# Kernel optimization log

Hardware: AMD Instinct MI355X
Metric: run time of the kernel (lower is better)

## Reference

```python
import jax, jax.numpy as jnp
import numpy as np

NEG_SLOPE = 0.2


def _gat_layer(x, src, dst, W, att_src, att_dst, bias, concat):
    # x: [N, Fin], W: [Fin, H*C], att_*: [H, C], bias: [H*C] or [C]
    N = x.shape[0]
    H, C = att_src.shape
    h = (x @ W).reshape(N, H, C)                      # node features per head
    a_src = jnp.sum(h * att_src, axis=-1)             # [N, H]
    a_dst = jnp.sum(h * att_dst, axis=-1)             # [N, H]
    e = jax.nn.leaky_relu(a_src[src] + a_dst[dst], NEG_SLOPE)  # [E, H]
    # segment softmax over destination nodes
    m = jax.ops.segment_max(e, dst, num_segments=N)   # [N, H]
    m = jnp.where(jnp.isfinite(m), m, 0.0)
    ex = jnp.exp(e - m[dst])
    s = jax.ops.segment_sum(ex, dst, num_segments=N)  # [N, H]
    alpha = ex / (s[dst] + 1e-16)                     # [E, H]
    msg = h[src] * alpha[:, :, None]                  # [E, H, C]
    out = jax.ops.segment_sum(msg, dst, num_segments=N)  # [N, H, C]
    out = out.reshape(N, H * C) if concat else out.mean(axis=1)
    return out + bias


def setup_inputs() -> dict:
    key = jax.random.key(0)
    ks = jax.random.split(key, 20)
    N, E, Fin, Cg, H = 50000, 800000, 128, 64, 4
    HC = H * Cg
    s = 0.1
    x = jax.random.normal(ks[0], (N, Fin), jnp.float32)
    edge_index = jax.random.randint(ks[1], (2, E), 0, N, dtype=jnp.int32)
    inp = {
        'x': x,
        'edge_index': edge_index,
        'W0': jax.random.normal(ks[2], (Fin, HC), jnp.float32) * s,
        'as0': jax.random.normal(ks[3], (H, Cg), jnp.float32) * s,
        'ad0': jax.random.normal(ks[4], (H, Cg), jnp.float32) * s,
        'b0': jnp.zeros((HC,), jnp.float32),
        'W1': jax.random.normal(ks[5], (HC, HC), jnp.float32) * s,
        'as1': jax.random.normal(ks[6], (H, Cg), jnp.float32) * s,
        'ad1': jax.random.normal(ks[7], (H, Cg), jnp.float32) * s,
        'b1': jnp.zeros((HC,), jnp.float32),
        'W2': jax.random.normal(ks[8], (HC, HC), jnp.float32) * s,
        'as2': jax.random.normal(ks[9], (H, Cg), jnp.float32) * s,
        'ad2': jax.random.normal(ks[10], (H, Cg), jnp.float32) * s,
        'b2': jnp.zeros((Cg,), jnp.float32),
        # linear head: 64 -> 128 -> 10
        'lw0': jax.random.normal(ks[11], (Cg, 128), jnp.float32) * s,
        'lb0': jnp.zeros((128,), jnp.float32),
        'lw1': jax.random.normal(ks[12], (128, 10), jnp.float32) * s,
        'lb1': jnp.zeros((10,), jnp.float32),
    }
    return inp


def reference(x, edge_index, W0, as0, ad0, b0, W1, as1, ad1, b1,
              W2, as2, ad2, b2, lw0, lb0, lw1, lb1):
    N = x.shape[0]
    # PyG GATConv add_self_loops=True: append self-loop edges
    loop = jnp.arange(N, dtype=edge_index.dtype)
    src = jnp.concatenate([edge_index[0], loop])
    dst = jnp.concatenate([edge_index[1], loop])
    h = _gat_layer(x, src, dst, W0, as0, ad0, b0, True)
    h = _gat_layer(h, src, dst, W1, as1, ad1, b1, True)
    h = _gat_layer(h, src, dst, W2, as2, ad2, b2, False)
    h = jax.nn.relu(h @ lw0 + lb0)
    return h @ lw1 + lb1
```

## Files before the change

kernel.cpp:

```cpp
#include <hip/hip_runtime.h>
#include <hip/hip_bf16.h>

#define HEADS 4
#define CH 64
#define HC 256

typedef __attribute__((ext_vector_type(8))) short short8;
typedef __attribute__((ext_vector_type(4))) float f32x4;
typedef __attribute__((ext_vector_type(8))) _Float16 half8;

__device__ inline unsigned short f2bf(float f){
  unsigned u = __float_as_uint(f);
  return (unsigned short)((u + 0x7FFF + ((u >> 16) & 1)) >> 16);
}


__global__ void hist_kernel(const int* __restrict__ dst, int E, int ET, int* __restrict__ cnt){
  int e = blockIdx.x * blockDim.x + threadIdx.x;
  if (e >= ET) return;
  int d = (e < E) ? dst[e] : (e - E);
  atomicAdd(&cnt[d], 1);
}

__global__ void blocksum_kernel(const int* __restrict__ cnt, int N, int* __restrict__ bsum){
  int tid = threadIdx.x;
  int i = blockIdx.x * 256 + tid;
  int v = (i < N) ? cnt[i] : 0;
  #pragma unroll
  for (int off = 32; off >= 1; off >>= 1) v += __shfl_xor(v, off);
  __shared__ int ws[4];
  if ((tid & 63) == 0) ws[tid >> 6] = v;
  __syncthreads();
  if (tid == 0) bsum[blockIdx.x] = ws[0] + ws[1] + ws[2] + ws[3];
}

__global__ void scanb_kernel(int* __restrict__ bsum, int nb){
  __shared__ int buf[256];
  int tid = threadIdx.x;
  int v = (tid < nb) ? bsum[tid] : 0;
  buf[tid] = v;
  __syncthreads();
  #pragma unroll
  for (int off = 1; off < 256; off <<= 1){
    int t = (tid >= off) ? buf[tid - off] : 0;
    __syncthreads();
    buf[tid] += t;
    __syncthreads();
  }
  if (tid < nb) bsum[tid] = buf[tid] - v;
}

__global__ void scanfinal_kernel(const int* __restrict__ cnt, const int* __restrict__ bsum,
                                 int* __restrict__ ptr, int* __restrict__ cur, int N){
  __shared__ int buf[256];
  int tid = threadIdx.x;
  int i = blockIdx.x * 256 + tid;
  int v = (i < N) ? cnt[i] : 0;
  buf[tid] = v;
  __syncthreads();
  #pragma unroll
  for (int off = 1; off < 256; off <<= 1){
    int t = (tid >= off) ? buf[tid - off] : 0;
    __syncthreads();
    buf[tid] += t;
    __syncthreads();
  }
  int exc = buf[tid] - v + bsum[blockIdx.x];
  if (i < N){
    ptr[i] = exc; cur[i] = exc;
    if (i == N - 1) ptr[N] = exc + v;
  }
}

__global__ void scatter_kernel(const int* __restrict__ src, const int* __restrict__ dst,
                               int E, int ET, int* __restrict__ cur,
                               int* __restrict__ csr_src, int* __restrict__ csr_dst){
  int e = blockIdx.x * blockDim.x + threadIdx.x;
  if (e >= ET) return;
  int s, d;
  if (e < E){ s = src[e]; d = dst[e]; } else { s = e - E; d = e - E; }
  int pos = atomicAdd(&cur[d], 1);
  csr_src[pos] = s;
  csr_dst[pos] = d;
}


__global__ void dhist_kernel(const int* __restrict__ cnt, int N, int* __restrict__ dbins){
  __shared__ int lb[64];
  int tid = threadIdx.x;
  if (tid < 64) lb[tid] = 0;
  __syncthreads();
  int n = blockIdx.x * 256 + tid;
  if (n < N) atomicAdd(&lb[min(cnt[n], 63)], 1);
  __syncthreads();
  if (tid < 64 && lb[tid]) atomicAdd(&dbins[tid], lb[tid]);
}

__global__ void dscan_kernel(int* __restrict__ dbins, int* __restrict__ dcur){
  int lane = threadIdx.x;
  int v = dbins[lane];
  int s = v;
  #pragma unroll
  for (int off = 1; off < 64; off <<= 1){
    int t = __shfl_up(s, off);
    if (lane >= off) s += t;
  }
  int exc = s - v;
  dbins[lane] = exc;
  dcur[lane] = exc;
}

__global__ void dscatter_kernel(const int* __restrict__ cnt, int N, int* __restrict__ dcur,
                                int* __restrict__ perm){
  __shared__ int lb[64];
  __shared__ int base[64];
  int tid = threadIdx.x;
  if (tid < 64) lb[tid] = 0;
  __syncthreads();
  int n = blockIdx.x * 256 + tid;
  bool valid = n < N;
  int bin = 0, rank = 0;
  if (valid){
    bin = min(cnt[n], 63);
    rank = atomicAdd(&lb[bin], 1);
  }
  __syncthreads();
  if (tid < 64) base[tid] = lb[tid] ? atomicAdd(&dcur[tid], lb[tid]) : 0;
  __syncthreads();
  if (valid) perm[base[bin] + rank] = n;
}


__global__ void ew_kernel(const int* __restrict__ csr_src, const int* __restrict__ csr_dst,
                          const float* __restrict__ a_src, const float* __restrict__ a_dst,
                          float* __restrict__ w, int ET){
  int i = blockIdx.x * 256 + threadIdx.x;
  if (i >= ET) return;
  int s = csr_src[i], d = csr_dst[i];
  float4 as = *(const float4*)&a_src[(size_t)s * 4];
  float4 ad = *(const float4*)&a_dst[(size_t)d * 4];
  float4 r;
  float e;
  e = as.x + ad.x; e = e > 0.f ? e : 0.2f * e; r.x = __expf(e);
  e = as.y + ad.y; e = e > 0.f ? e : 0.2f * e; r.y = __expf(e);
  e = as.z + ad.z; e = e > 0.f ? e : 0.2f * e; r.z = __expf(e);
  e = as.w + ad.w; e = e > 0.f ? e : 0.2f * e; r.w = __expf(e);
  *(float4*)&w[(size_t)i * 4] = r;
}


__global__ void wsplit_kernel(const float* __restrict__ W0, unsigned short* __restrict__ h0,
                              unsigned short* __restrict__ l0,
                              const float* __restrict__ W1, unsigned short* __restrict__ h1,
                              unsigned short* __restrict__ l1,
                              const float* __restrict__ W2, unsigned short* __restrict__ h2,
                              unsigned short* __restrict__ l2){
  int idx = blockIdx.x * 256 + threadIdx.x;
  const float* W; unsigned short *hi, *lo; int K;
  if (idx < 128 * HC){ W = W0; hi = h0; lo = l0; K = 128; }
  else if (idx < (128 + 256) * HC){ idx -= 128 * HC; W = W1; hi = h1; lo = l1; K = 256; }
  else { idx -= (128 + 256) * HC; W = W2; hi = h2; lo = l2; K = 256; }
  int k = idx >> 8, n = idx & 255;
  float w = W[idx];
  unsigned short hb = f2bf(w);
  float hf = __uint_as_float((unsigned)hb << 16);
  unsigned short lb = f2bf(w - hf);
  hi[(size_t)n * K + k] = hb;
  lo[(size_t)n * K + k] = lb;
}


__global__ void xsplit_kernel(const float* __restrict__ x, int total4,
                              unsigned short* __restrict__ xhi, unsigned short* __restrict__ xlo){
  int i4 = blockIdx.x * 256 + threadIdx.x;
  if (i4 >= total4) return;
  float4 v = *(const float4*)&x[(size_t)i4 * 4];
  float va[4] = {v.x, v.y, v.z, v.w};
  unsigned short h4[4], l4[4];
  #pragma unroll
  for (int j = 0; j < 4; j++){
    unsigned short hb = f2bf(va[j]);
    float hf = __uint_as_float((unsigned)hb << 16);
    h4[j] = hb;
    l4[j] = f2bf(va[j] - hf);
  }
  *(ushort4*)&xhi[(size_t)i4 * 4] = make_ushort4(h4[0], h4[1], h4[2], h4[3]);
  *(ushort4*)&xlo[(size_t)i4 * 4] = make_ushort4(l4[0], l4[1], l4[2], l4[3]);
}


__global__ void lwsplit_kernel(const float* __restrict__ lw0,
                               unsigned short* __restrict__ l0hi, unsigned short* __restrict__ l0lo,
                               const float* __restrict__ lw1, _Float16* __restrict__ l1T){
  int idx = blockIdx.x * 256 + threadIdx.x;
  if (idx < 8192){
    int n = idx & 127, k = idx >> 7;
    float w = lw0[k * 128 + n];
    unsigned short hb = f2bf(w);
    float hf = __uint_as_float((unsigned)hb << 16);
    unsigned short lb = f2bf(w - hf);
    l0hi[n * 64 + k] = hb;
    l0lo[n * 64 + k] = lb;
  } else if (idx < 8192 + 2048){
    int id = idx - 8192;
    int n = id & 15, k = id >> 4;
    float w = (n < 10) ? lw1[k * 10 + n] : 0.f;
    l1T[n * 128 + k] = (_Float16)w;
  }
}


__launch_bounds__(256, 2)
__global__ void gemm_mfma_kernel(const unsigned short* __restrict__ Ahi,
                                 const unsigned short* __restrict__ Alo,
                                 const unsigned short* __restrict__ BhiT,
                                 const unsigned short* __restrict__ BloT,
                                 _Float16* __restrict__ Cm,
                                 const float* __restrict__ att_s, const float* __restrict__ att_d,
                                 float* __restrict__ a_src, float* __restrict__ a_dst,
                                 int K){
  __shared__ unsigned short As_hi[128][40];
  __shared__ unsigned short As_lo[128][40];
  __shared__ unsigned short Bs_hi[128][40];
  __shared__ unsigned short Bs_lo[128][40];

  int tid = threadIdx.x;
  int m0 = blockIdx.x * 128, n0 = blockIdx.y * 128;
  int wave = tid >> 6, lane = tid & 63;
  int wm = (wave >> 1) * 64, wn = (wave & 1) * 64;
  int col = lane & 15, quad = lane >> 4;

  int mS = tid >> 2, q8 = (tid & 3) * 8;
  size_t baseA0 = (size_t)(m0 + mS) * K + q8;
  size_t baseA1 = (size_t)(m0 + mS + 64) * K + q8;
  size_t baseB0 = (size_t)(n0 + mS) * K + q8;
  size_t baseB1 = (size_t)(n0 + mS + 64) * K + q8;

  short8 pA[4], pB[4];
  pA[0] = *(const short8*)&Ahi[baseA0];  pA[1] = *(const short8*)&Alo[baseA0];
  pA[2] = *(const short8*)&Ahi[baseA1];  pA[3] = *(const short8*)&Alo[baseA1];
  pB[0] = *(const short8*)&BhiT[baseB0]; pB[1] = *(const short8*)&BloT[baseB0];
  pB[2] = *(const short8*)&BhiT[baseB1]; pB[3] = *(const short8*)&BloT[baseB1];

  f32x4 acc[4][4];
  #pragma unroll
  for (int a = 0; a < 4; a++)
    #pragma unroll
    for (int b = 0; b < 4; b++)
      acc[a][b] = (f32x4){0.f, 0.f, 0.f, 0.f};

  for (int k0 = 0; k0 < K; k0 += 32){
    __syncthreads();
    *(short8*)&As_hi[mS][q8]      = pA[0];
    *(short8*)&As_lo[mS][q8]      = pA[1];
    *(short8*)&As_hi[mS + 64][q8] = pA[2];
    *(short8*)&As_lo[mS + 64][q8] = pA[3];
    *(short8*)&Bs_hi[mS][q8]      = pB[0];
    *(short8*)&Bs_lo[mS][q8]      = pB[1];
    *(short8*)&Bs_hi[mS + 64][q8] = pB[2];
    *(short8*)&Bs_lo[mS + 64][q8] = pB[3];
    __syncthreads();

    if (k0 + 32 < K){
      size_t o = (size_t)(k0 + 32);
      pA[0] = *(const short8*)&Ahi[baseA0 + o];  pA[1] = *(const short8*)&Alo[baseA0 + o];
      pA[2] = *(const short8*)&Ahi[baseA1 + o];  pA[3] = *(const short8*)&Alo[baseA1 + o];
      pB[0] = *(const short8*)&BhiT[baseB0 + o]; pB[1] = *(const short8*)&BloT[baseB0 + o];
      pB[2] = *(const short8*)&BhiT[baseB1 + o]; pB[3] = *(const short8*)&BloT[baseB1 + o];
    }

    short8 af[4][2], bf[4][2];
    #pragma unroll
    for (int t = 0; t < 4; t++){
      af[t][0] = *(const short8*)&As_hi[wm + t * 16 + col][quad * 8];
      af[t][1] = *(const short8*)&As_lo[wm + t * 16 + col][quad * 8];
      bf[t][0] = *(const short8*)&Bs_hi[wn + t * 16 + col][quad * 8];
      bf[t][1] = *(const short8*)&Bs_lo[wn + t * 16 + col][quad * 8];
    }
    #pragma unroll
    for (int mt = 0; mt < 4; mt++)
      #pragma unroll
      for (int nt = 0; nt < 4; nt++){
        acc[mt][nt] = __builtin_amdgcn_mfma_f32_16x16x32_bf16(af[mt][0], bf[nt][0], acc[mt][nt], 0, 0, 0);
        acc[mt][nt] = __builtin_amdgcn_mfma_f32_16x16x32_bf16(af[mt][1], bf[nt][0], acc[mt][nt], 0, 0, 0);
        acc[mt][nt] = __builtin_amdgcn_mfma_f32_16x16x32_bf16(af[mt][0], bf[nt][1], acc[mt][nt], 0, 0, 0);
      }
  }

  #pragma unroll
  for (int mt = 0; mt < 4; mt++)
    #pragma unroll
    for (int nt = 0; nt < 4; nt++){
      int colg = n0 + wn + nt * 16 + col;
      #pragma unroll
      for (int r = 0; r < 4; r++){
        int row = m0 + wm + mt * 16 + quad * 4 + r;
        Cm[(size_t)row * HC + colg] = (_Float16)acc[mt][nt][r];
      }
    }

  int head = (n0 + wn) >> 6;
  float asv[4], adv[4];
  #pragma unroll
  for (int nt = 0; nt < 4; nt++){
    asv[nt] = att_s[head * CH + nt * 16 + col];
    adv[nt] = att_d[head * CH + nt * 16 + col];
  }
  #pragma unroll
  for (int mt = 0; mt < 4; mt++){
    float sp[4] = {0.f,0.f,0.f,0.f}, dp[4] = {0.f,0.f,0.f,0.f};
    #pragma unroll
    for (int nt = 0; nt < 4; nt++)
      #pragma unroll
      for (int r = 0; r < 4; r++){
        sp[r] += acc[mt][nt][r] * asv[nt];
        dp[r] += acc[mt][nt][r] * adv[nt];
      }
    #pragma unroll
    for (int off = 1; off <= 8; off <<= 1)
      #pragma unroll
      for (int r = 0; r < 4; r++){
        sp[r] += __shfl_xor(sp[r], off);
        dp[r] += __shfl_xor(dp[r], off);
      }
    if (col == 0){
      #pragma unroll
      for (int r = 0; r < 4; r++){
        int row = m0 + wm + mt * 16 + quad * 4 + r;
        a_src[row * HEADS + head] = sp[r];
        a_dst[row * HEADS + head] = dp[r];
      }
    }
  }
}


__global__ void agg_kernel(const _Float16* __restrict__ h, const float* __restrict__ w,
                           const int* __restrict__ ptr, const int* __restrict__ csr_src,
                           const int* __restrict__ perm,
                           const float* __restrict__ bias,
                           unsigned short* __restrict__ out_hi, unsigned short* __restrict__ out_lo,
                           int mean_mode, const float* __restrict__ b2,
                           float* __restrict__ f2){
  __shared__ float sm[HEADS][8][CH];
  int head = threadIdx.x >> 6;
  int lane = threadIdx.x & 63;
  int slot = lane >> 3, c8 = lane & 7;
  int pn = perm[blockIdx.x * 8 + slot];
  int beg = 0, deg = 0;
  if (pn >= 0){ beg = ptr[pn]; deg = ptr[pn + 1] - beg; }

  int maxdeg = deg;
  #pragma unroll
  for (int off = 8; off <= 32; off <<= 1) maxdeg = max(maxdeg, __shfl_xor(maxdeg, off));

  float acc[8] = {0.f,0.f,0.f,0.f,0.f,0.f,0.f,0.f};
  float ss = 0.f;
  #pragma unroll 2
  for (int it = 0; it < maxdeg; ++it){
    bool valid = it < deg;
    int idx = beg + (valid ? it : 0);
    int s = csr_src[idx];
    float wv = w[(size_t)idx * 4 + head];
    wv = valid ? wv : 0.f;
    half8 hv = *(const half8*)&h[(size_t)s * HC + head * CH + c8 * 8];
    #pragma unroll
    for (int j = 0; j < 8; j++) acc[j] += wv * (float)hv[j];
    ss += wv;
  }
  float inv = 1.f / (ss + 1e-16f);
  #pragma unroll
  for (int j = 0; j < 8; j++) acc[j] *= inv;

  if (!mean_mode){
    if (pn >= 0){
      const float* bp = &bias[head * CH + c8 * 8];
      short8 hi8, lo8;
      #pragma unroll
      for (int j = 0; j < 8; j++){
        float v = acc[j] + bp[j];
        unsigned short hb = f2bf(v);
        float hf = __uint_as_float((unsigned)hb << 16);
        hi8[j] = (short)hb;
        lo8[j] = (short)f2bf(v - hf);
      }
      size_t o = (size_t)pn * HC + head * CH + c8 * 8;
      *(short8*)&out_hi[o] = hi8;
      *(short8*)&out_lo[o] = lo8;
    }
  } else {
    #pragma unroll
    for (int j = 0; j < 8; j++) sm[head][slot][c8 * 8 + j] = acc[j];
    __syncthreads();
    for (int t = threadIdx.x; t < 512; t += 256){
      int sl = t >> 6, ch = t & 63;
      int pn2 = perm[blockIdx.x * 8 + sl];
      if (pn2 >= 0)
        f2[(size_t)pn2 * CH + ch] =
          0.25f * (sm[0][sl][ch] + sm[1][sl][ch] + sm[2][sl][ch] + sm[3][sl][ch]) + b2[ch];
    }
  }
}


__launch_bounds__(256, 2)
__global__ void head_mfma_kernel(const float* __restrict__ f2,
                                 const unsigned short* __restrict__ lw0hiT,
                                 const unsigned short* __restrict__ lw0loT,
                                 const _Float16* __restrict__ lw1T,
                                 const float* __restrict__ lb0,
                                 const float* __restrict__ lb1,
                                 float* __restrict__ outp, int N){
  __shared__ __align__(16) unsigned short L[27648];
  __shared__ __align__(16) _Float16 Ls[16][136];
  const int tid = threadIdx.x;
  const int wave = tid >> 6, lane = tid & 63;
  const int col = lane & 15, quad = lane >> 4;
  const int m0 = blockIdx.x * 64;

  { int n = tid >> 4, k = (tid & 15) * 8;
    *(half8*)&Ls[n][k] = *(const half8*)&lw1T[n * 128 + k]; }

  #pragma unroll
  for (int r = 0; r < 2; r++){
    int id = r * 256 + tid;
    int m = id >> 3, q = id & 7;
    int gm = m0 + m;
    float va[8];
    if (gm < N){
      float4 v0 = *(const float4*)&f2[(size_t)gm * CH + q * 8];
      float4 v1 = *(const float4*)&f2[(size_t)gm * CH + q * 8 + 4];
      va[0]=v0.x; va[1]=v0.y; va[2]=v0.z; va[3]=v0.w;
      va[4]=v1.x; va[5]=v1.y; va[6]=v1.z; va[7]=v1.w;
    } else {
      #pragma unroll
      for (int j = 0; j < 8; j++) va[j] = 0.f;
    }
    short8 hi8, lo8;
    #pragma unroll
    for (int j = 0; j < 8; j++){
      unsigned short hb = f2bf(va[j]);
      float hf = __uint_as_float((unsigned)hb << 16);
      hi8[j] = (short)hb;
      lo8[j] = (short)f2bf(va[j] - hf);
    }
    *(short8*)&L[m * 72 + q * 8] = hi8;
    *(short8*)&L[4608 + m * 72 + q * 8] = lo8;
  }
  #pragma unroll
  for (int r = 0; r < 4; r++){
    int id = r * 256 + tid;
    int n = id >> 3, q = id & 7;
    *(short8*)&L[9216 + n * 72 + q * 8]  = *(const short8*)&lw0hiT[n * 64 + q * 8];
    *(short8*)&L[18432 + n * 72 + q * 8] = *(const short8*)&lw0loT[n * 64 + q * 8];
  }
  __syncthreads();

  const int wn = wave * 32;
  f32x4 acc[4][2];
  #pragma unroll
  for (int a = 0; a < 4; a++)
    #pragma unroll
    for (int b = 0; b < 2; b++) acc[a][b] = (f32x4){0.f,0.f,0.f,0.f};

  #pragma unroll
  for (int ks = 0; ks < 2; ks++){
    int k = ks * 32 + quad * 8;
    short8 ah[4], al[4], bh[2], bl[2];
    #pragma unroll
    for (int mt = 0; mt < 4; mt++){
      ah[mt] = *(short8*)&L[(mt * 16 + col) * 72 + k];
      al[mt] = *(short8*)&L[4608 + (mt * 16 + col) * 72 + k];
    }
    #pragma unroll
    for (int nt = 0; nt < 2; nt++){
      bh[nt] = *(short8*)&L[9216 + (wn + nt * 16 + col) * 72 + k];
      bl[nt] = *(short8*)&L[18432 + (wn + nt * 16 + col) * 72 + k];
    }
    #pragma unroll
    for (int mt = 0; mt < 4; mt++)
      #pragma unroll
      for (int nt = 0; nt < 2; nt++){
        acc[mt][nt] = __builtin_amdgcn_mfma_f32_16x16x32_bf16(ah[mt], bh[nt], acc[mt][nt], 0, 0, 0);
        acc[mt][nt] = __builtin_amdgcn_mfma_f32_16x16x32_bf16(al[mt], bh[nt], acc[mt][nt], 0, 0, 0);
        acc[mt][nt] = __builtin_amdgcn_mfma_f32_16x16x32_bf16(ah[mt], bl[nt], acc[mt][nt], 0, 0, 0);
      }
  }
  __syncthreads();

  _Float16* Zp = (_Float16*)L;
  #pragma unroll
  for (int nt = 0; nt < 2; nt++){
    int n = wn + nt * 16 + col;
    float b = lb0[n];
    #pragma unroll
    for (int mt = 0; mt < 4; mt++)
      #pragma unroll
      for (int r2 = 0; r2 < 4; r2++){
        int m = mt * 16 + quad * 4 + r2;
        float z = acc[mt][nt][r2] + b;
        Zp[m * 136 + n] = (_Float16)fmaxf(z, 0.f);
      }
  }
  __syncthreads();

  f32x4 acc2 = (f32x4){0.f,0.f,0.f,0.f};
  #pragma unroll
  for (int ks = 0; ks < 4; ks++){
    int k = ks * 32 + quad * 8;
    half8 a2 = *(half8*)&Zp[(wave * 16 + col) * 136 + k];
    half8 b2v = *(half8*)&Ls[col][k];
    acc2 = __builtin_amdgcn_mfma_f32_16x16x32_f16(a2, b2v, acc2, 0, 0, 0);
  }
  if (col < 10){
    float bb = lb1[col];
    #pragma unroll
    for (int r2 = 0; r2 < 4; r2++){
      int row = m0 + wave * 16 + quad * 4 + r2;
      if (row < N) outp[(size_t)row * 10 + col] = acc2[r2] + bb;
    }
  }
}


extern "C" void kernel_launch(void* const* d_in, const int* in_sizes, int n_in,
                              void* d_out, int out_size, void* d_ws, size_t ws_size,
                              hipStream_t stream) {
  const float* x   = (const float*)d_in[0];
  const int*   ei  = (const int*)d_in[1];
  const float* W0  = (const float*)d_in[2];
  const float* as0 = (const float*)d_in[3];
  const float* ad0 = (const float*)d_in[4];
  const float* b0  = (const float*)d_in[5];
  const float* W1  = (const float*)d_in[6];
  const float* as1 = (const float*)d_in[7];
  const float* ad1 = (const float*)d_in[8];
  const float* b1  = (const float*)d_in[9];
  const float* W2  = (const float*)d_in[10];
  const float* as2 = (const float*)d_in[11];
  const float* ad2 = (const float*)d_in[12];
  const float* b2  = (const float*)d_in[13];
  const float* lw0 = (const float*)d_in[14];
  const float* lb0 = (const float*)d_in[15];
  const float* lw1 = (const float*)d_in[16];
  const float* lb1 = (const float*)d_in[17];
  float* outp = (float*)d_out;

  int N  = in_sizes[0] / 128;
  int E  = in_sizes[1] / 2;
  int ET = E + N;
  int nb = (N + 255) / 256;
  int Mp = ((N + 127) / 128) * 128;
  int Np8 = ((N + 7) / 8) * 8;

  char* ws = (char*)d_ws;
  _Float16* Hb = (_Float16*)ws;       ws += (size_t)Mp * HC * sizeof(_Float16);
  unsigned short* Fhi = (unsigned short*)ws; ws += (size_t)Mp * HC * 2;
  unsigned short* Flo = (unsigned short*)ws; ws += (size_t)Mp * HC * 2;
  float* f2  = (float*)ws; ws += (size_t)N * CH * sizeof(float);
  float* a_s = (float*)ws; ws += (size_t)Mp * HEADS * sizeof(float);
  float* a_d = (float*)ws; ws += (size_t)Mp * HEADS * sizeof(float);
  float* ewt = (float*)ws; ws += (size_t)ET * HEADS * sizeof(float);
  int* cnt   = (int*)ws;   ws += (size_t)N * sizeof(int);
  int* cur   = (int*)ws;   ws += (size_t)N * sizeof(int);
  int* ptrA  = (int*)ws;   ws += (size_t)(N + 1) * sizeof(int);
  int* bsum  = (int*)ws;   ws += (size_t)nb * sizeof(int);
  int* csr   = (int*)ws;   ws += (size_t)ET * sizeof(int);
  int* csrd  = (int*)ws;   ws += (size_t)ET * sizeof(int);
  int* perm  = (int*)ws;   ws += (size_t)Np8 * sizeof(int);
  int* dbins = (int*)ws;   ws += 64 * sizeof(int);
  int* dcur  = (int*)ws;   ws += 64 * sizeof(int);
  unsigned short* w0hi = (unsigned short*)ws; ws += (size_t)128 * HC * 2;
  unsigned short* w0lo = (unsigned short*)ws; ws += (size_t)128 * HC * 2;
  unsigned short* w1hi = (unsigned short*)ws; ws += (size_t)HC * HC * 2;
  unsigned short* w1lo = (unsigned short*)ws; ws += (size_t)HC * HC * 2;
  unsigned short* w2hi = (unsigned short*)ws; ws += (size_t)HC * HC * 2;
  unsigned short* w2lo = (unsigned short*)ws; ws += (size_t)HC * HC * 2;
  unsigned short* l0hi = (unsigned short*)ws; ws += (size_t)8192 * 2;
  unsigned short* l0lo = (unsigned short*)ws; ws += (size_t)8192 * 2;
  _Float16* l1T        = (_Float16*)ws;       ws += (size_t)2048 * 2;

  const int* srcArr = ei;
  const int* dstArr = ei + E;

  hipMemsetAsync(cnt, 0, (size_t)N * sizeof(int), stream);
  hipMemsetAsync(dbins, 0, 64 * sizeof(int), stream);
  hipMemsetAsync(perm, 0xFF, (size_t)Np8 * sizeof(int), stream);
  hist_kernel<<<(ET + 255) / 256, 256, 0, stream>>>(dstArr, E, ET, cnt);
  blocksum_kernel<<<nb, 256, 0, stream>>>(cnt, N, bsum);
  scanb_kernel<<<1, 256, 0, stream>>>(bsum, nb);
  scanfinal_kernel<<<nb, 256, 0, stream>>>(cnt, bsum, ptrA, cur, N);
  scatter_kernel<<<(ET + 255) / 256, 256, 0, stream>>>(srcArr, dstArr, E, ET, cur, csr, csrd);

  dhist_kernel<<<nb, 256, 0, stream>>>(cnt, N, dbins);
  dscan_kernel<<<1, 64, 0, stream>>>(dbins, dcur);
  dscatter_kernel<<<nb, 256, 0, stream>>>(cnt, N, dcur, perm);

  wsplit_kernel<<<((128 + 256 + 256) * HC) / 256, 256, 0, stream>>>(
      W0, w0hi, w0lo, W1, w1hi, w1lo, W2, w2hi, w2lo);
  lwsplit_kernel<<<(8192 + 2048 + 255) / 256, 256, 0, stream>>>(lw0, l0hi, l0lo, lw1, l1T);
  xsplit_kernel<<<(N * 128 / 4 + 255) / 256, 256, 0, stream>>>(x, N * 128 / 4, Fhi, Flo);

  dim3 ggrid(Mp / 128, 2);
  int eb = (ET + 255) / 256;
  int ab = Np8 / 8;

  gemm_mfma_kernel<<<ggrid, 256, 0, stream>>>(Fhi, Flo, w0hi, w0lo, Hb, as0, ad0, a_s, a_d, 128);
  ew_kernel<<<eb, 256, 0, stream>>>(csr, csrd, a_s, a_d, ewt, ET);
  agg_kernel<<<ab, 256, 0, stream>>>(Hb, ewt, ptrA, csr, perm, b0, Fhi, Flo, 0, nullptr, nullptr);

  gemm_mfma_kernel<<<ggrid, 256, 0, stream>>>(Fhi, Flo, w1hi, w1lo, Hb, as1, ad1, a_s, a_d, HC);
  ew_kernel<<<eb, 256, 0, stream>>>(csr, csrd, a_s, a_d, ewt, ET);
  agg_kernel<<<ab, 256, 0, stream>>>(Hb, ewt, ptrA, csr, perm, b1, Fhi, Flo, 0, nullptr, nullptr);

  gemm_mfma_kernel<<<ggrid, 256, 0, stream>>>(Fhi, Flo, w2hi, w2lo, Hb, as2, ad2, a_s, a_d, HC);
  ew_kernel<<<eb, 256, 0, stream>>>(csr, csrd, a_s, a_d, ewt, ET);
  agg_kernel<<<ab, 256, 0, stream>>>(Hb, ewt, ptrA, csr, perm, nullptr, nullptr, nullptr, 1, b2, f2);

  head_mfma_kernel<<<(N + 63) / 64, 256, 0, stream>>>(f2, l0hi, l0lo, l1T, lb0, lb1, outp, N);
}
```

Before: 577.1 us.

## Sort CSR neighbor lists per node and unroll aggregation gather by four

Adds a per-node insertion sort of source indices within each CSR segment after the scatter step, so neighbor gathers during aggregation visit increasing addresses and may get better cache locality. The aggregation loop is also manually unrolled by four, issuing four index, weight and feature loads before accumulating, which exposes more memory-level parallelism. The sort adds a kernel whose cost depends on degree (average about 17), and it reorders csr_src without reordering csr_dst. That is harmless only because every edge in a segment shares the same destination, but the edge weights computed later follow the sorted order.

Result: slower. 665.2 us (+15.3%).

```diff
diff --git a/kernel.cpp b/kernel.cpp
--- a/kernel.cpp
+++ b/kernel.cpp
@@ -82,6 +82,19 @@
   int pos = atomicAdd(&cur[d], 1);
   csr_src[pos] = s;
   csr_dst[pos] = d;
+}
+
+
+__global__ void esort_kernel(const int* __restrict__ ptr, int* __restrict__ csr, int N){
+  int n = blockIdx.x * 256 + threadIdx.x;
+  if (n >= N) return;
+  int beg = ptr[n], end = ptr[n + 1];
+  for (int i = beg + 1; i < end; i++){
+    int v = csr[i];
+    int j = i - 1;
+    while (j >= beg && csr[j] > v){ csr[j + 1] = csr[j]; j--; }
+    csr[j + 1] = v;
+  }
 }
 
 
@@ -356,13 +369,35 @@
 
   float acc[8] = {0.f,0.f,0.f,0.f,0.f,0.f,0.f,0.f};
   float ss = 0.f;
-  #pragma unroll 2
-  for (int it = 0; it < maxdeg; ++it){
+  int it = 0;
+  for (; it + 4 <= maxdeg; it += 4){
+    int idx[4]; float wv[4];
+    #pragma unroll
+    for (int k = 0; k < 4; k++)
+      idx[k] = beg + ((it + k < deg) ? it + k : 0);
+    int s0 = csr_src[idx[0]], s1 = csr_src[idx[1]];
+    int s2 = csr_src[idx[2]], s3 = csr_src[idx[3]];
+    #pragma unroll
+    for (int k = 0; k < 4; k++)
+      wv[k] = (it + k < deg) ? w[(size_t)idx[k] * 4 + head] : 0.f;
+    half8 h0 = *(const half8*)&h[(size_t)s0 * HC + head * CH + c8 * 8];
+    half8 h1 = *(const half8*)&h[(size_t)s1 * HC + head * CH + c8 * 8];
+    half8 h2 = *(const half8*)&h[(size_t)s2 * HC + head * CH + c8 * 8];
+    half8 h3 = *(const half8*)&h[(size_t)s3 * HC + head * CH + c8 * 8];
+    #pragma unroll
+    for (int j = 0; j < 8; j++){
+      acc[j] += wv[0] * (float)h0[j];
+      acc[j] += wv[1] * (float)h1[j];
+      acc[j] += wv[2] * (float)h2[j];
+      acc[j] += wv[3] * (float)h3[j];
+    }
+    ss += wv[0] + wv[1] + wv[2] + wv[3];
+  }
+  for (; it < maxdeg; ++it){
     bool valid = it < deg;
     int idx = beg + (valid ? it : 0);
     int s = csr_src[idx];
-    float wv = w[(size_t)idx * 4 + head];
-    wv = valid ? wv : 0.f;
+    float wv = valid ? w[(size_t)idx * 4 + head] : 0.f;
     half8 hv = *(const half8*)&h[(size_t)s * HC + head * CH + c8 * 8];
     #pragma unroll
     for (int j = 0; j < 8; j++) acc[j] += wv * (float)hv[j];
@@ -591,6 +626,7 @@
   scanb_kernel<<<1, 256, 0, stream>>>(bsum, nb);
   scanfinal_kernel<<<nb, 256, 0, stream>>>(cnt, bsum, ptrA, cur, N);
   scatter_kernel<<<(ET + 255) / 256, 256, 0, stream>>>(srcArr, dstArr, E, ET, cur, csr, csrd);
+  esort_kernel<<<nb, 256, 0, stream>>>(ptrA, csr, N);
 
   dhist_kernel<<<nb, 256, 0, stream>>>(cnt, N, dbins);
   dscan_kernel<<<1, 64, 0, stream>>>(dbins, dcur);
```
